# Kernel optimization log

Measured on AMD Instinct MI355X. Metric: run time of the kernel, lower is better.

## Reference

```python
import jax, jax.numpy as jnp
import numpy as np

N_NODES = 50000


def _gcn_norm(edge_index, n):
    # Add self-loops (PyG GCNConv default) and compute symmetric normalization.
    src = jnp.concatenate([edge_index[0], jnp.arange(n, dtype=edge_index.dtype)])
    dst = jnp.concatenate([edge_index[1], jnp.arange(n, dtype=edge_index.dtype)])
    deg = jax.ops.segment_sum(jnp.ones(src.shape[0], dtype=jnp.float32), dst,
                              num_segments=n)
    dinv = jnp.where(deg > 0, jax.lax.rsqrt(deg), 0.0)
    norm = dinv[src] * dinv[dst]  # [E+N]
    return src, dst, norm


def _gcn_conv(x, src, dst, norm, W, b, n):
    h = x @ W                              # [N, out] linear transform first
    msgs = h[src] * norm[:, None]          # gather + edge-wise scale [E+N, out]
    out = jax.ops.segment_sum(msgs, dst, num_segments=n)  # scatter-add
    return out + b


def setup_inputs() -> dict:
    key = jax.random.key(0)
    k1, k2, k3, k4 = jax.random.split(key, 4)
    N, E, F, H, C = N_NODES, 1600000, 128, 128, 64
    x = jax.random.normal(k1, (N, F), dtype=jnp.float32)
    edge_index = jax.random.randint(k2, (2, E), 0, N, dtype=jnp.int64)
    W1 = jax.random.normal(k3, (F, H), dtype=jnp.float32) * 0.05
    b1 = jnp.zeros((H,), dtype=jnp.float32)
    W2 = jax.random.normal(k4, (H, C), dtype=jnp.float32) * 0.05
    b2 = jnp.zeros((C,), dtype=jnp.float32)
    return {"x": x, "edge_index": edge_index, "W1": W1, "b1": b1,
            "W2": W2, "b2": b2}


def reference(x, edge_index, W1, b1, W2, b2):
    n = x.shape[0]
    src, dst, norm = _gcn_norm(edge_index, n)
    h = _gcn_conv(x, src, dst, norm, W1, b1, n)
    h = jax.nn.relu(h)
    out = _gcn_conv(h, src, dst, norm, W2, b2, n)
    return out
```

## Files before the change

### kernel.cpp

```cpp
#include <hip/hip_runtime.h>
#include <hip/hip_bf16.h>
#include <stdint.h>

#define N_NODES 50000
#define N_EDGES 1600000
#define N_TOT   (N_EDGES + N_NODES)
#define NBKT      256
#define BKT_NODES 196
#define BKT_CAP   7168
#define PBKT_CAP  9216
#define TILE      4096
#define EPT       16
#define ZROW      N_NODES
#define PLANE_E   1600032

typedef unsigned short u16;
typedef __attribute__((ext_vector_type(8))) short short8;
typedef __attribute__((ext_vector_type(4))) float floatx4;
typedef __attribute__((ext_vector_type(2))) float f2;

__device__ __forceinline__ float b2f(u16 u) {
    union { unsigned int i; float f; } v; v.i = ((unsigned int)u) << 16; return v.f;
}
__device__ __forceinline__ float asf(unsigned u) {
    union { unsigned int i; float f; } v; v.i = u; return v.f;
}
__device__ __forceinline__ u16 f2b(float f) {
    union { unsigned int i; float f; } v; v.f = f;
    unsigned int r = (v.i + 0x7FFFu + ((v.i >> 16) & 1u)) >> 16;
    return (u16)r;
}

__device__ __forceinline__ void accu(f2& a, unsigned u) {
    f2 r; r.x = asf(u << 16); r.y = asf(u & 0xFFFF0000u);
    a += r;
}
__device__ __forceinline__ void acc4u(f2* a, uint4 q) {
    accu(a[0], q.x); accu(a[1], q.y); accu(a[2], q.z); accu(a[3], q.w);
}

__global__ __launch_bounds__(256) void k_part(const int* __restrict__ ei,
                                              const unsigned* __restrict__ xw,
                                              int* __restrict__ flags,
                                              unsigned* __restrict__ pairs,
                                              int* __restrict__ bktcnt) {
    __shared__ unsigned pairsL[TILE];
    __shared__ unsigned char bktL[TILE];
    __shared__ int hist[NBKT], incl[NBKT], delta[NBKT];
    __shared__ int zc, pc;
    int tid = threadIdx.x;
    long base = (long)blockIdx.x * TILE;
    hist[tid] = 0;
    if (tid == 0) { zc = 0; pc = 0; }
    __syncthreads();
    unsigned hw = ((const unsigned*)ei)[2 * tid + 1];
    atomicAdd(&zc, hw == 0 ? 1 : 0);
    if (blockIdx.x == 0) {
        unsigned w = xw[tid];
        int ex = (w >> 7) & 0xFF;
        atomicAdd(&pc, ((ex == 0) || (ex >= 0x60 && ex <= 0x9F)) ? 1 : 0);
    }
    __syncthreads();
    int i64 = zc > 250;
    if (blockIdx.x == 0 && tid == 0) {
        flags[0] = (pc < 160) ? 1 : 0;
        flags[1] = i64;
    }

    int myb[EPT], myrank[EPT]; unsigned myp[EPT];
#pragma unroll
    for (int t = 0; t < EPT; t++) {
        long idx = base + t * 256 + tid;
        int b = -1; unsigned p = 0;
        if (idx < N_TOT) {
            int s, d;
            if (idx < N_EDGES) {
                if (i64) { s = ei[2 * idx]; d = ei[2 * (N_EDGES + idx)]; }
                else     { s = ei[idx];     d = ei[N_EDGES + idx]; }
            } else {
                s = d = (int)(idx - N_EDGES);
            }
            b = d / BKT_NODES;
            p = (unsigned)s | ((unsigned)(d - b * BKT_NODES) << 16);
        }
        myb[t] = b; myp[t] = p;
        myrank[t] = (b >= 0) ? atomicAdd(&hist[b], 1) : 0;
    }
    __syncthreads();

    int tot = hist[tid];
    incl[tid] = tot;
    __syncthreads();
    for (int o = 1; o < NBKT; o <<= 1) {
        int t2 = (tid >= o) ? incl[tid - o] : 0;
        __syncthreads();
        incl[tid] += t2;
        __syncthreads();
    }
    int excl = incl[tid] - tot;
    int gb = atomicAdd(&bktcnt[tid], tot);
    hist[tid]  = excl;
    delta[tid] = tid * BKT_CAP + gb - excl;
    __syncthreads();

#pragma unroll
    for (int t = 0; t < EPT; t++) {
        if (myb[t] >= 0) {
            int slot = hist[myb[t]] + myrank[t];
            pairsL[slot] = myp[t];
            bktL[slot]   = (unsigned char)myb[t];
        }
    }
    __syncthreads();
    int count = incl[NBKT - 1];
    for (int i = tid; i < count; i += 256) {
        int b = bktL[i];
        int pos = delta[b] + i;
        if (pos - b * BKT_CAP < BKT_CAP)
            pairs[pos] = pairsL[i];
    }
}

__global__ __launch_bounds__(256) void k_bucket(const unsigned* __restrict__ pairs,
                                                const int* __restrict__ bktcnt,
                                                int* __restrict__ rowstart,
                                                int* __restrict__ deg,
                                                float* __restrict__ dinv,
                                                u16* __restrict__ csr) {
    __shared__ u16 csrL[PBKT_CAP];
    __shared__ int degL[NBKT], curL[NBKT], scanT[NBKT];
    int b = blockIdx.x, tid = threadIdx.x;
    int cnt = bktcnt[b];
    const unsigned* reg = pairs + (size_t)b * BKT_CAP;
    degL[tid] = 0;
    __syncthreads();
    for (int i = tid; i < cnt; i += 256)
        atomicAdd(&degL[reg[i] >> 16], 1);
    __syncthreads();
    int n = b * BKT_NODES + tid;
    int valid = (tid < BKT_NODES) && (n < N_NODES);
    int v = degL[tid];
    int pv = valid ? ((v + 15) & ~15) : 0;
    scanT[tid] = pv;
    __syncthreads();
    for (int o = 1; o < NBKT; o <<= 1) {
        int t = (tid >= o) ? scanT[tid - o] : 0;
        __syncthreads();
        scanT[tid] += t;
        __syncthreads();
    }
    int pexcl = scanT[tid] - pv;
    curL[tid] = pexcl;
    if (valid) {
        rowstart[n] = b * PBKT_CAP + pexcl;
        deg[n]      = v;
        dinv[n]     = rsqrtf((float)v);
    }
    int pcnt = scanT[NBKT - 1];
    if (pcnt > PBKT_CAP) pcnt = PBKT_CAP;
    __syncthreads();
    for (int i = tid; i < pcnt; i += 256) csrL[i] = (u16)ZROW;
    __syncthreads();
    for (int i = tid; i < cnt; i += 256) {
        unsigned p = reg[i];
        int slot = atomicAdd(&curL[p >> 16], 1);
        if (slot < PBKT_CAP) csrL[slot] = (u16)(p & 0xFFFFu);
    }
    __syncthreads();
    for (int i = tid; i < pcnt; i += 256)
        csr[(size_t)b * PBKT_CAP + i] = csrL[i];
}

template<int NOUT, bool ADYN, bool APLANE>
__global__ __launch_bounds__(256) void k_gemm(const void* __restrict__ A,
                                              const void* __restrict__ W,
                                              const float* __restrict__ dinv,
                                              u16* __restrict__ out, int M,
                                              const int* __restrict__ flags) {
    const int isf32 = flags[0];
    constexpr int LDW = 136;
    __shared__ __align__(16) u16 Wt[NOUT * LDW];
    int tid = threadIdx.x;
    if (blockIdx.x == 0 && tid < NOUT)
        out[(size_t)(tid >> 5) * PLANE_E + (size_t)M * 32 + (tid & 31)] = 0;
    const float* Wf = (const float*)W;
    const u16*   Wu = (const u16*)W;
    for (int idx = tid; idx < 128 * NOUT; idx += 256) {
        int k = idx / NOUT, n = idx % NOUT;
        Wt[n * LDW + k] = isf32 ? f2b(Wf[idx]) : Wu[idx];
    }
    __syncthreads();

    int wave = tid >> 6, lane = tid & 63;
    int quad = lane >> 4, l16 = lane & 15;
    int r0 = blockIdx.x * 64 + wave * 16;
    int r = r0 + l16; if (r >= M) r = M - 1;

    floatx4 acc[NOUT / 16];
#pragma unroll
    for (int i = 0; i < NOUT / 16; i++) acc[i] = (floatx4)(0.f);

#pragma unroll
    for (int ks = 0; ks < 4; ks++) {
        short8 a;
        if (ADYN && isf32) {
            const float* af = (const float*)A + (size_t)r * 128 + ks * 32 + quad * 8;
            float4 v0 = ((const float4*)af)[0];
            float4 v1 = ((const float4*)af)[1];
            a[0] = (short)f2b(v0.x); a[1] = (short)f2b(v0.y);
            a[2] = (short)f2b(v0.z); a[3] = (short)f2b(v0.w);
            a[4] = (short)f2b(v1.x); a[5] = (short)f2b(v1.y);
            a[6] = (short)f2b(v1.z); a[7] = (short)f2b(v1.w);
        } else if (APLANE) {
            a = *(const short8*)((const u16*)A + (size_t)ks * PLANE_E
                                 + (size_t)r * 32 + quad * 8);
        } else {
            a = ((const short8*)((const u16*)A + (size_t)r * 128))[ks * 4 + quad];
        }
#pragma unroll
        for (int nt = 0; nt < NOUT / 16; nt++) {
            const short8* bp = (const short8*)&Wt[(nt * 16 + l16) * LDW + ks * 32 + quad * 8];
            acc[nt] = __builtin_amdgcn_mfma_f32_16x16x32_bf16(a, *bp, acc[nt], 0, 0, 0);
        }
    }
    float sc[4];
#pragma unroll
    for (int j = 0; j < 4; j++) {
        int row = r0 + quad * 4 + j;
        sc[j] = dinv[row < M ? row : 0];
    }
#pragma unroll
    for (int nt = 0; nt < NOUT / 16; nt++) {
#pragma unroll
        for (int j = 0; j < 4; j++) {
            int row = r0 + quad * 4 + j;
            if (row < M)
                out[(size_t)(nt >> 1) * PLANE_E + (size_t)row * 32
                    + (nt & 1) * 16 + l16] = f2b(acc[nt][j] * sc[j]);
        }
    }
}

__global__ __launch_bounds__(256) void k_agg1(const u16* __restrict__ h,
                                              const u16* __restrict__ csr,
                                              const int* __restrict__ rowstart,
                                              const int* __restrict__ deg,
                                              const float* __restrict__ dinv,
                                              const void* __restrict__ bias,
                                              u16* __restrict__ out,
                                              const int* __restrict__ flags) {
    int wave = threadIdx.x >> 6, lane = threadIdx.x & 63;
    int bid = blockIdx.x;
    int xcd = bid & 7;
    int s = xcd >> 1;
    int d = (xcd & 1) * 25000 + (bid >> 3) * 4 + wave;
    int grp = lane >> 2, lg = lane & 3;
    int start = rowstart[d], dg = deg[d];
    int R = (dg + 15) >> 4;
    const u16* cp = csr + start + grp;
    const char* hB = (const char*)(h + (size_t)s * PLANE_E);
    unsigned lb = (unsigned)lg << 4;

    f2 acc[4] = {};
    int rl = R - 1;
    unsigned i0 = cp[0];
    unsigned i1 = cp[(unsigned)((1 <= rl ? 1 : rl) << 4)];
    uint4 q0 = *(const uint4*)(hB + ((i0 << 6) + lb));
    uint4 q1 = *(const uint4*)(hB + ((i1 << 6) + lb));
    for (int r = 0; r < R - 2; r++) {
        int rn = (r + 2 <= rl) ? (r + 2) : rl;
        unsigned i2 = cp[(unsigned)(rn << 4)];
        acc4u(acc, q0);
        q0 = q1;
        q1 = *(const uint4*)(hB + ((i2 << 6) + lb));
    }
    acc4u(acc, q0);
    if (R >= 2) acc4u(acc, q1);

#pragma unroll
    for (int j = 0; j < 4; j++) {
        acc[j].x += __shfl_xor(acc[j].x, 4);  acc[j].y += __shfl_xor(acc[j].y, 4);
        acc[j].x += __shfl_xor(acc[j].x, 8);  acc[j].y += __shfl_xor(acc[j].y, 8);
        acc[j].x += __shfl_xor(acc[j].x, 16); acc[j].y += __shfl_xor(acc[j].y, 16);
        acc[j].x += __shfl_xor(acc[j].x, 32); acc[j].y += __shfl_xor(acc[j].y, 32);
    }
    if (grp == 0) {
        int isf32 = flags[0];
        float dd = dinv[d];
        int fb = s * 32 + lg * 8;
        u16 r8[8];
#pragma unroll
        for (int j = 0; j < 4; j++) {
            float bx = isf32 ? ((const float*)bias)[fb + 2 * j]
                             : b2f(((const u16*)bias)[fb + 2 * j]);
            float by = isf32 ? ((const float*)bias)[fb + 2 * j + 1]
                             : b2f(((const u16*)bias)[fb + 2 * j + 1]);
            float vx = acc[j].x * dd + bx;
            float vy = acc[j].y * dd + by;
            r8[2 * j]     = f2b(vx > 0.f ? vx : 0.f);
            r8[2 * j + 1] = f2b(vy > 0.f ? vy : 0.f);
        }
        uint4 o;
        o.x = r8[0] | ((unsigned)r8[1] << 16); o.y = r8[2] | ((unsigned)r8[3] << 16);
        o.z = r8[4] | ((unsigned)r8[5] << 16); o.w = r8[6] | ((unsigned)r8[7] << 16);
        *(uint4*)(out + (size_t)s * PLANE_E + (size_t)d * 32 + lg * 8) = o;
    }
}

__global__ __launch_bounds__(256) void k_agg2(const u16* __restrict__ h,
                                              const u16* __restrict__ csr,
                                              const int* __restrict__ rowstart,
                                              const int* __restrict__ deg,
                                              const float* __restrict__ dinv,
                                              const void* __restrict__ bias,
                                              float* __restrict__ out,
                                              const int* __restrict__ flags) {
    int wave = threadIdx.x >> 6, lane = threadIdx.x & 63;
    int bid = blockIdx.x;
    int xcd = bid & 7;
    int s = xcd >> 2;
    int d = (xcd & 3) * 12500 + (bid >> 3) * 4 + wave;
    int grp = lane >> 2, lg = lane & 3;
    int start = rowstart[d], dg = deg[d];
    int R = (dg + 15) >> 4;
    const u16* cp = csr + start + grp;
    const char* hB = (const char*)(h + (size_t)s * PLANE_E);
    unsigned lb = (unsigned)lg << 4;

    f2 acc[4] = {};
    int rl = R - 1;
    unsigned i0 = cp[0];
    unsigned i1 = cp[(unsigned)((1 <= rl ? 1 : rl) << 4)];
    uint4 q0 = *(const uint4*)(hB + ((i0 << 6) + lb));
    uint4 q1 = *(const uint4*)(hB + ((i1 << 6) + lb));
    for (int r = 0; r < R - 2; r++) {
        int rn = (r + 2 <= rl) ? (r + 2) : rl;
        unsigned i2 = cp[(unsigned)(rn << 4)];
        acc4u(acc, q0);
        q0 = q1;
        q1 = *(const uint4*)(hB + ((i2 << 6) + lb));
    }
    acc4u(acc, q0);
    if (R >= 2) acc4u(acc, q1);

#pragma unroll
    for (int j = 0; j < 4; j++) {
        acc[j].x += __shfl_xor(acc[j].x, 4);  acc[j].y += __shfl_xor(acc[j].y, 4);
        acc[j].x += __shfl_xor(acc[j].x, 8);  acc[j].y += __shfl_xor(acc[j].y, 8);
        acc[j].x += __shfl_xor(acc[j].x, 16); acc[j].y += __shfl_xor(acc[j].y, 16);
        acc[j].x += __shfl_xor(acc[j].x, 32); acc[j].y += __shfl_xor(acc[j].y, 32);
    }
    if (grp == 0) {
        int isf32 = flags[0];
        float dd = dinv[d];
        int fb = s * 32 + lg * 8;
        float r8[8];
#pragma unroll
        for (int j = 0; j < 4; j++) {
            float bx = isf32 ? ((const float*)bias)[fb + 2 * j]
                             : b2f(((const u16*)bias)[fb + 2 * j]);
            float by = isf32 ? ((const float*)bias)[fb + 2 * j + 1]
                             : b2f(((const u16*)bias)[fb + 2 * j + 1]);
            r8[2 * j]     = acc[j].x * dd + bx;
            r8[2 * j + 1] = acc[j].y * dd + by;
        }
        float4* op = (float4*)(out + (size_t)d * 64 + fb);
        op[0] = make_float4(r8[0], r8[1], r8[2], r8[3]);
        op[1] = make_float4(r8[4], r8[5], r8[6], r8[7]);
    }
}

extern "C" void kernel_launch(void* const* d_in, const int* in_sizes, int n_in,
                              void* d_out, int out_size, void* d_ws, size_t ws_size,
                              hipStream_t stream) {
    const void* x  = d_in[0];
    const int*  ei = (const int*)d_in[1];
    const void* W1 = d_in[2];
    const void* b1 = d_in[3];
    const void* W2 = d_in[4];
    const void* b2 = d_in[5];
    float* out = (float*)d_out;

    char* ws = (char*)d_ws;
    int*      flags    = (int*)(ws + 0);
    int*      bktcnt   = (int*)(ws + 1024);
    int*      deg      = (int*)(ws + 4096);
    int*      rowstart = (int*)(ws + 204800);
    float*    dinv     = (float*)(ws + 405504);
    u16*      csr      = (u16*)(ws + 606208);
    unsigned* pairs    = (unsigned*)(ws + 5324800);
    u16*      h1       = (u16*)(ws + 5324800);
    u16*      out1     = (u16*)(ws + 18125056);
    u16*      h2       = (u16*)(ws + 5324800);

    hipMemsetAsync(bktcnt, 0, NBKT * sizeof(int), stream);
    k_part   <<<(N_TOT + TILE - 1) / TILE, 256, 0, stream>>>(ei, (const unsigned*)x,
                                                             flags, pairs, bktcnt);
    k_bucket <<<NBKT, 256, 0, stream>>>(pairs, bktcnt, rowstart, deg, dinv, csr);

    k_gemm<128, true, false> <<<(N_NODES + 63) / 64, 256, 0, stream>>>(x, W1, dinv, h1, N_NODES, flags);
    k_agg1<<<50000, 256, 0, stream>>>(h1, csr, rowstart, deg, dinv, b1, out1, flags);
    k_gemm<64, false, true> <<<(N_NODES + 63) / 64, 256, 0, stream>>>(out1, W2, dinv, h2, N_NODES, flags);
    k_agg2<<<25000, 256, 0, stream>>>(h2, csr, rowstart, deg, dinv, b2, out, flags);
}
```

Baseline: 278.7 us.

## Assign one node per 4-lane group in aggregation with 8-padded vector CSR reads

The aggregation kernels move from one wave per destination node, with 16 lane groups splitting its edges and a shuffle reduction, to one 4-lane group per node that walks its own CSR row in 16-byte chunks of eight indices. The grid shrinks to match. CSR rows are padded to multiples of 8 instead of 16, which cuts wasted zero-row gathers. The bucket kernel also uses vectorised loads and stores with nontemporal hints. The change removes the cross-lane reductions and most padding work. In exchange, per-node degree imbalance now falls inside a wave, and the gathers lose the two-deep software prefetch.

```diff
diff --git a/kernel.cpp b/kernel.cpp
--- a/kernel.cpp
+++ b/kernel.cpp
@@ -8,7 +8,7 @@
 #define NBKT      256
 #define BKT_NODES 196
 #define BKT_CAP   7168
-#define PBKT_CAP  9216
+#define PBKT_CAP  8192
 #define TILE      4096
 #define EPT       16
 #define ZROW      N_NODES
@@ -18,6 +18,8 @@
 typedef __attribute__((ext_vector_type(8))) short short8;
 typedef __attribute__((ext_vector_type(4))) float floatx4;
 typedef __attribute__((ext_vector_type(2))) float f2;
+typedef __attribute__((ext_vector_type(4))) unsigned u32x4;
+typedef __attribute__((ext_vector_type(4))) float f32x4;
 
 __device__ __forceinline__ float b2f(u16 u) {
     union { unsigned int i; float f; } v; v.i = ((unsigned int)u) << 16; return v.f;
@@ -35,8 +37,11 @@
     f2 r; r.x = asf(u << 16); r.y = asf(u & 0xFFFF0000u);
     a += r;
 }
-__device__ __forceinline__ void acc4u(f2* a, uint4 q) {
+__device__ __forceinline__ void acc4u(f2* a, u32x4 q) {
     accu(a[0], q.x); accu(a[1], q.y); accu(a[2], q.z); accu(a[3], q.w);
+}
+__device__ __forceinline__ u32x4 g64(const char* hB, unsigned i, unsigned lb) {
+    return *(const u32x4*)(hB + ((i << 6) + lb));
 }
 
 __global__ __launch_bounds__(256) void k_part(const int* __restrict__ ei,
@@ -117,7 +122,7 @@
         int b = bktL[i];
         int pos = delta[b] + i;
         if (pos - b * BKT_CAP < BKT_CAP)
-            pairs[pos] = pairsL[i];
+            __builtin_nontemporal_store(pairsL[i], &pairs[pos]);
     }
 }
 
@@ -127,20 +132,27 @@
                                                 int* __restrict__ deg,
                                                 float* __restrict__ dinv,
                                                 u16* __restrict__ csr) {
-    __shared__ u16 csrL[PBKT_CAP];
+    __shared__ __align__(16) u16 csrL[PBKT_CAP];
     __shared__ int degL[NBKT], curL[NBKT], scanT[NBKT];
     int b = blockIdx.x, tid = threadIdx.x;
     int cnt = bktcnt[b];
     const unsigned* reg = pairs + (size_t)b * BKT_CAP;
     degL[tid] = 0;
     __syncthreads();
-    for (int i = tid; i < cnt; i += 256)
-        atomicAdd(&degL[reg[i] >> 16], 1);
+    int cnt4 = cnt & ~3;
+    for (int i = tid * 4; i < cnt4; i += 1024) {
+        u32x4 p4 = __builtin_nontemporal_load((const u32x4*)(reg + i));
+        atomicAdd(&degL[p4.x >> 16], 1);
+        atomicAdd(&degL[p4.y >> 16], 1);
+        atomicAdd(&degL[p4.z >> 16], 1);
+        atomicAdd(&degL[p4.w >> 16], 1);
+    }
+    { int i = cnt4 + tid; if (i < cnt) atomicAdd(&degL[reg[i] >> 16], 1); }
     __syncthreads();
     int n = b * BKT_NODES + tid;
     int valid = (tid < BKT_NODES) && (n < N_NODES);
     int v = degL[tid];
-    int pv = valid ? ((v + 15) & ~15) : 0;
+    int pv = valid ? ((v + 7) & ~7) : 0;
     scanT[tid] = pv;
     __syncthreads();
     for (int o = 1; o < NBKT; o <<= 1) {
@@ -159,16 +171,32 @@
     int pcnt = scanT[NBKT - 1];
     if (pcnt > PBKT_CAP) pcnt = PBKT_CAP;
     __syncthreads();
-    for (int i = tid; i < pcnt; i += 256) csrL[i] = (u16)ZROW;
-    __syncthreads();
-    for (int i = tid; i < cnt; i += 256) {
-        unsigned p = reg[i];
-        int slot = atomicAdd(&curL[p >> 16], 1);
-        if (slot < PBKT_CAP) csrL[slot] = (u16)(p & 0xFFFFu);
-    }
-    __syncthreads();
-    for (int i = tid; i < pcnt; i += 256)
-        csr[(size_t)b * PBKT_CAP + i] = csrL[i];
+    {
+        u32x4 zfill;
+        zfill.x = zfill.y = zfill.z = zfill.w = ((unsigned)ZROW << 16) | (unsigned)ZROW;
+        for (int i = tid * 8; i < pcnt; i += 2048)
+            *(u32x4*)(csrL + i) = zfill;
+    }
+    __syncthreads();
+    for (int i = tid * 4; i < cnt4; i += 1024) {
+        u32x4 p4 = __builtin_nontemporal_load((const u32x4*)(reg + i));
+        int s0 = atomicAdd(&curL[p4.x >> 16], 1); if (s0 < PBKT_CAP) csrL[s0] = (u16)p4.x;
+        int s1 = atomicAdd(&curL[p4.y >> 16], 1); if (s1 < PBKT_CAP) csrL[s1] = (u16)p4.y;
+        int s2 = atomicAdd(&curL[p4.z >> 16], 1); if (s2 < PBKT_CAP) csrL[s2] = (u16)p4.z;
+        int s3 = atomicAdd(&curL[p4.w >> 16], 1); if (s3 < PBKT_CAP) csrL[s3] = (u16)p4.w;
+    }
+    {
+        int i = cnt4 + tid;
+        if (i < cnt) {
+            unsigned p = reg[i];
+            int slot = atomicAdd(&curL[p >> 16], 1);
+            if (slot < PBKT_CAP) csrL[slot] = (u16)p;
+        }
+    }
+    __syncthreads();
+    for (int i = tid * 8; i < pcnt; i += 2048)
+        __builtin_nontemporal_store(*(const u32x4*)(csrL + i),
+                                    (u32x4*)(csr + (size_t)b * PBKT_CAP + i));
 }
 
 template<int NOUT, bool ADYN, bool APLANE>
@@ -250,41 +278,31 @@
                                               u16* __restrict__ out,
                                               const int* __restrict__ flags) {
     int wave = threadIdx.x >> 6, lane = threadIdx.x & 63;
-    int bid = blockIdx.x;
-    int xcd = bid & 7;
-    int s = xcd >> 1;
-    int d = (xcd & 1) * 25000 + (bid >> 3) * 4 + wave;
+    int xcd = blockIdx.x & 7;
+    int s = xcd >> 1, half = xcd & 1;
     int grp = lane >> 2, lg = lane & 3;
-    int start = rowstart[d], dg = deg[d];
-    int R = (dg + 15) >> 4;
-    const u16* cp = csr + start + grp;
+    int off = (blockIdx.x >> 3) * 64 + wave * 16 + grp;
+    int act = off < 25000;
+    int d = half * 25000 + (act ? off : 0);
+    int start = rowstart[d];
+    int R8 = act ? ((deg[d] + 7) >> 3) : 0;
+    const u32x4* cp = (const u32x4*)(csr + start);
     const char* hB = (const char*)(h + (size_t)s * PLANE_E);
     unsigned lb = (unsigned)lg << 4;
 
     f2 acc[4] = {};
-    int rl = R - 1;
-    unsigned i0 = cp[0];
-    unsigned i1 = cp[(unsigned)((1 <= rl ? 1 : rl) << 4)];
-    uint4 q0 = *(const uint4*)(hB + ((i0 << 6) + lb));
-    uint4 q1 = *(const uint4*)(hB + ((i1 << 6) + lb));
-    for (int r = 0; r < R - 2; r++) {
-        int rn = (r + 2 <= rl) ? (r + 2) : rl;
-        unsigned i2 = cp[(unsigned)(rn << 4)];
-        acc4u(acc, q0);
-        q0 = q1;
-        q1 = *(const uint4*)(hB + ((i2 << 6) + lb));
-    }
-    acc4u(acc, q0);
-    if (R >= 2) acc4u(acc, q1);
-
-#pragma unroll
-    for (int j = 0; j < 4; j++) {
-        acc[j].x += __shfl_xor(acc[j].x, 4);  acc[j].y += __shfl_xor(acc[j].y, 4);
-        acc[j].x += __shfl_xor(acc[j].x, 8);  acc[j].y += __shfl_xor(acc[j].y, 8);
-        acc[j].x += __shfl_xor(acc[j].x, 16); acc[j].y += __shfl_xor(acc[j].y, 16);
-        acc[j].x += __shfl_xor(acc[j].x, 32); acc[j].y += __shfl_xor(acc[j].y, 32);
-    }
-    if (grp == 0) {
+    for (int k = 0; k < R8; k++) {
+        u32x4 ci = __builtin_nontemporal_load(cp + k);
+        acc4u(acc, g64(hB, ci.x & 0xFFFFu, lb));
+        acc4u(acc, g64(hB, ci.x >> 16, lb));
+        acc4u(acc, g64(hB, ci.y & 0xFFFFu, lb));
+        acc4u(acc, g64(hB, ci.y >> 16, lb));
+        acc4u(acc, g64(hB, ci.z & 0xFFFFu, lb));
+        acc4u(acc, g64(hB, ci.z >> 16, lb));
+        acc4u(acc, g64(hB, ci.w & 0xFFFFu, lb));
+        acc4u(acc, g64(hB, ci.w >> 16, lb));
+    }
+    if (act) {
         int isf32 = flags[0];
         float dd = dinv[d];
         int fb = s * 32 + lg * 8;
@@ -300,10 +318,11 @@
             r8[2 * j]     = f2b(vx > 0.f ? vx : 0.f);
             r8[2 * j + 1] = f2b(vy > 0.f ? vy : 0.f);
         }
-        uint4 o;
+        u32x4 o;
         o.x = r8[0] | ((unsigned)r8[1] << 16); o.y = r8[2] | ((unsigned)r8[3] << 16);
         o.z = r8[4] | ((unsigned)r8[5] << 16); o.w = r8[6] | ((unsigned)r8[7] << 16);
-        *(uint4*)(out + (size_t)s * PLANE_E + (size_t)d * 32 + lg * 8) = o;
+        __builtin_nontemporal_store(o,
+            (u32x4*)(out + (size_t)s * PLANE_E + (size_t)d * 32 + lg * 8));
     }
 }
 
@@ -316,41 +335,31 @@
                                               float* __restrict__ out,
                                               const int* __restrict__ flags) {
     int wave = threadIdx.x >> 6, lane = threadIdx.x & 63;
-    int bid = blockIdx.x;
-    int xcd = bid & 7;
-    int s = xcd >> 2;
-    int d = (xcd & 3) * 12500 + (bid >> 3) * 4 + wave;
+    int xcd = blockIdx.x & 7;
+    int s = xcd >> 2, quarter = xcd & 3;
     int grp = lane >> 2, lg = lane & 3;
-    int start = rowstart[d], dg = deg[d];
-    int R = (dg + 15) >> 4;
-    const u16* cp = csr + start + grp;
+    int off = (blockIdx.x >> 3) * 64 + wave * 16 + grp;
+    int act = off < 12500;
+    int d = quarter * 12500 + (act ? off : 0);
+    int start = rowstart[d];
+    int R8 = act ? ((deg[d] + 7) >> 3) : 0;
+    const u32x4* cp = (const u32x4*)(csr + start);
     const char* hB = (const char*)(h + (size_t)s * PLANE_E);
     unsigned lb = (unsigned)lg << 4;
 
     f2 acc[4] = {};
-    int rl = R - 1;
-    unsigned i0 = cp[0];
-    unsigned i1 = cp[(unsigned)((1 <= rl ? 1 : rl) << 4)];
-    uint4 q0 = *(const uint4*)(hB + ((i0 << 6) + lb));
-    uint4 q1 = *(const uint4*)(hB + ((i1 << 6) + lb));
-    for (int r = 0; r < R - 2; r++) {
-        int rn = (r + 2 <= rl) ? (r + 2) : rl;
-        unsigned i2 = cp[(unsigned)(rn << 4)];
-        acc4u(acc, q0);
-        q0 = q1;
-        q1 = *(const uint4*)(hB + ((i2 << 6) + lb));
-    }
-    acc4u(acc, q0);
-    if (R >= 2) acc4u(acc, q1);
-
-#pragma unroll
-    for (int j = 0; j < 4; j++) {
-        acc[j].x += __shfl_xor(acc[j].x, 4);  acc[j].y += __shfl_xor(acc[j].y, 4);
-        acc[j].x += __shfl_xor(acc[j].x, 8);  acc[j].y += __shfl_xor(acc[j].y, 8);
-        acc[j].x += __shfl_xor(acc[j].x, 16); acc[j].y += __shfl_xor(acc[j].y, 16);
-        acc[j].x += __shfl_xor(acc[j].x, 32); acc[j].y += __shfl_xor(acc[j].y, 32);
-    }
-    if (grp == 0) {
+    for (int k = 0; k < R8; k++) {
+        u32x4 ci = __builtin_nontemporal_load(cp + k);
+        acc4u(acc, g64(hB, ci.x & 0xFFFFu, lb));
+        acc4u(acc, g64(hB, ci.x >> 16, lb));
+        acc4u(acc, g64(hB, ci.y & 0xFFFFu, lb));
+        acc4u(acc, g64(hB, ci.y >> 16, lb));
+        acc4u(acc, g64(hB, ci.z & 0xFFFFu, lb));
+        acc4u(acc, g64(hB, ci.z >> 16, lb));
+        acc4u(acc, g64(hB, ci.w & 0xFFFFu, lb));
+        acc4u(acc, g64(hB, ci.w >> 16, lb));
+    }
+    if (act) {
         int isf32 = flags[0];
         float dd = dinv[d];
         int fb = s * 32 + lg * 8;
@@ -364,9 +373,11 @@
             r8[2 * j]     = acc[j].x * dd + bx;
             r8[2 * j + 1] = acc[j].y * dd + by;
         }
-        float4* op = (float4*)(out + (size_t)d * 64 + fb);
-        op[0] = make_float4(r8[0], r8[1], r8[2], r8[3]);
-        op[1] = make_float4(r8[4], r8[5], r8[6], r8[7]);
+        float* op = out + (size_t)d * 64 + fb;
+        f32x4 o0; o0.x = r8[0]; o0.y = r8[1]; o0.z = r8[2]; o0.w = r8[3];
+        f32x4 o1; o1.x = r8[4]; o1.y = r8[5]; o1.z = r8[6]; o1.w = r8[7];
+        __builtin_nontemporal_store(o0, (f32x4*)op);
+        __builtin_nontemporal_store(o1, (f32x4*)op + 1);
     }
 }
 
@@ -399,7 +410,7 @@
     k_bucket <<<NBKT, 256, 0, stream>>>(pairs, bktcnt, rowstart, deg, dinv, csr);
 
     k_gemm<128, true, false> <<<(N_NODES + 63) / 64, 256, 0, stream>>>(x, W1, dinv, h1, N_NODES, flags);
-    k_agg1<<<50000, 256, 0, stream>>>(h1, csr, rowstart, deg, dinv, b1, out1, flags);
+    k_agg1<<<3128, 256, 0, stream>>>(h1, csr, rowstart, deg, dinv, b1, out1, flags);
     k_gemm<64, false, true> <<<(N_NODES + 63) / 64, 256, 0, stream>>>(out1, W2, dinv, h2, N_NODES, flags);
-    k_agg2<<<25000, 256, 0, stream>>>(h2, csr, rowstart, deg, dinv, b2, out, flags);
-}
+    k_agg2<<<1568, 256, 0, stream>>>(h2, csr, rowstart, deg, dinv, b2, out, flags);
+}
```

Result: faster. 242.9 us (-12.9%).
